# Optimization experiments

Measured on AMD Instinct MI355X. Metric: run time of the kernel, lower is better.

Reference implementation:

```python
import jax, jax.numpy as jnp
import numpy as np

D = 256        # d_model
DL = 256       # d_latent
S = 2048       # seq_len
B = 8          # batches
F = 8192       # facts per batch (padded)
MAXPOS = 4096
MAXPRED = 1024
NROLE = 64 + 2 # role_emb rows


def setup_inputs() -> dict:
    key = jax.random.key(0)
    ks = jax.random.split(key, 16)
    def nrm(k, shape, s=0.02):
        return jax.random.normal(k, shape, jnp.float32) * s
    return {
        "pos_emb": nrm(ks[0], (MAXPOS, D)),
        "pred_emb": nrm(ks[1], (MAXPRED, D)),
        "role_emb": nrm(ks[2], (NROLE, D)),
        "w1": nrm(ks[3], (3 * D, 2 * D)), "b1": jnp.zeros((2 * D,), jnp.float32),
        "w2": nrm(ks[4], (2 * D, D)),     "b2": jnp.zeros((D,), jnp.float32),
        "ln_g": jnp.ones((D,), jnp.float32), "ln_b": jnp.zeros((D,), jnp.float32),
        "lw1": nrm(ks[5], (D, DL)), "lb1": jnp.zeros((DL,), jnp.float32),
        "lw2": nrm(ks[6], (DL, DL)), "lb2": jnp.zeros((DL,), jnp.float32),
        "pred_idx": jax.random.randint(ks[7], (B, F), 0, MAXPRED),
        "a0": jax.random.randint(ks[8], (B, F), 0, S),
        "a1": jax.random.randint(ks[9], (B, F), 0, S),
        "role_idx": jax.random.randint(ks[10], (B, F), 0, NROLE),
        "is_role": jax.random.randint(ks[11], (B, F), 0, 2).astype(jnp.int32),
        "add_rev": jax.random.randint(ks[12], (B, F), 0, 2).astype(jnp.int32),
        "mask": jax.random.randint(ks[13], (B, F), 0, 2).astype(jnp.int32),
        "seq_len": S,
    }


def reference(pos_emb, pred_emb, role_emb, w1, b1, w2, b2, ln_g, ln_b,
              lw1, lb1, lw2, lb2,
              pred_idx, a0, a1, role_idx, is_role, add_rev, mask, seq_len):
    nodes = pos_emb[:seq_len]                 # [S, D] shared across batches
    pe = pred_emb[pred_idx]                   # [B, F, D]
    n0 = nodes[a0]                            # [B, F, D]
    n1 = nodes[a1]                            # [B, F, D]
    re = role_emb[role_idx]                   # [B, F, D]

    role_b = is_role.astype(bool)
    valid = mask.astype(bool)

    third = jnp.where(role_b[..., None], re, n1)
    x_fwd = jnp.concatenate([n0, pe, third], axis=-1)   # [B, F, 3D]
    x_rev = jnp.concatenate([n1, pe, n0], axis=-1)      # [B, F, 3D]

    def mlp(x):
        h = jax.nn.gelu(x @ w1 + b1, approximate=False)
        return h @ w2 + b2

    msg_fwd = mlp(x_fwd)                      # [B, F, D]
    msg_rev = mlp(x_rev)                      # [B, F, D]

    w_fwd = valid[..., None].astype(msg_fwd.dtype)
    w_rev = (valid & (~role_b) & add_rev.astype(bool))[..., None].astype(msg_rev.dtype)
    tgt_fwd = jnp.where(role_b, a0, a1)       # role msgs go to tok=a0, binary to a1

    def scat(msg, idx, w):
        return jax.ops.segment_sum(msg * w, idx, num_segments=seq_len)

    agg = jax.vmap(scat)(msg_fwd, tgt_fwd, w_fwd)
    agg = agg + jax.vmap(scat)(msg_rev, a0, w_rev)      # [B, S, D]

    x = nodes[None, :, :] + agg
    mu = jnp.mean(x, axis=-1, keepdims=True)
    var = jnp.mean(jnp.square(x - mu), axis=-1, keepdims=True)
    x = (x - mu) / jnp.sqrt(var + 1e-5) * ln_g + ln_b   # LayerNorm

    pooled = jnp.mean(x, axis=1)              # [B, D]
    h = jax.nn.gelu(pooled @ lw1 + lb1, approximate=False)
    return h @ lw2 + lb2                      # [B, DL]
```

## Files before the change

### kernel.cpp

```cpp
#include <hip/hip_runtime.h>
#include <hip/hip_bf16.h>
#include <cstdint>

#define S_LEN 2048
#define DIM   256
#define NBAT  8
#define NFE   8192
#define NEDGE (NBAT*NFE)
#define HID   512
#define INDIM 768

#define OFF_AGG   0u
#define OFF_POOL  16777216u
#define OFF_CNT   16785408u
#define OFF_NODES 16785664u
#define OFF_PRED  17834240u
#define OFF_ROLE  18358528u
#define OFF_W1P   18392576u
#define OFF_W2P   19179008u
#define OFF_FWD   19441152u
#define OFF_REV   19703296u
#define ZERO_BYTES 16785664u

typedef short bshort8 __attribute__((ext_vector_type(8)));
typedef float floatx4 __attribute__((ext_vector_type(4)));

__device__ __forceinline__ float gelu_f(float x) {
  return 0.5f * x * (1.0f + erff(x * 0.70710678118654752f));
}
__device__ __forceinline__ ushort f2bf(float v) {
  __hip_bfloat16 h = __float2bfloat16(v);
  return *reinterpret_cast<ushort*>(&h);
}

__global__ void prep_tables(const float* __restrict__ pos, const float* __restrict__ pred,
                            const float* __restrict__ role,
                            ushort* __restrict__ nodesT, ushort* __restrict__ predT,
                            ushort* __restrict__ roleT) {
  int i = blockIdx.x * blockDim.x + threadIdx.x;
  const int NN = S_LEN * DIM;
  const int NP = 1024 * DIM;
  if (i < NN) nodesT[i] = f2bf(pos[i]);
  else if (i < NN + NP) { int j = i - NN; predT[j] = f2bf(pred[j]); }
  else { int j = i - NN - NP; if (j < 66 * DIM) roleT[j] = f2bf(role[j]); }
}

__global__ void prep_w(const float* __restrict__ w1, const float* __restrict__ w2,
                       ushort* __restrict__ W1p, ushort* __restrict__ W2p) {
  int i = blockIdx.x * blockDim.x + threadIdx.x;
  const int N1 = INDIM * HID;
  if (i < N1) {
    int k = i >> 9, n = i & 511;
    W1p[(((k >> 3) << 9) + n) * 8 + (k & 7)] = f2bf(w1[i]);
  } else {
    int j = i - N1;
    int k = j >> 8, n = j & 255;
    W2p[(((k >> 3) << 8) + n) * 8 + (k & 7)] = f2bf(w2[j]);
  }
}

__global__ void build_lists(const int* __restrict__ mask, const int* __restrict__ is_role,
                            const int* __restrict__ add_rev,
                            int* __restrict__ fwd, int* __restrict__ rev, int* __restrict__ cnt) {
  int e = blockIdx.x * blockDim.x + threadIdx.x;
  if (e >= NEDGE) return;
  if (mask[e]) {
    int p = atomicAdd(&cnt[0], 1);
    fwd[p] = e;
    if (!is_role[e] && add_rev[e]) {
      int q = atomicAdd(&cnt[1], 1);
      rev[q] = e;
    }
  }
}

#define XSTR 1552
#define HSTR 1040
__global__ __launch_bounds__(512, 1)
void mlp_kernel(const int* __restrict__ cnt, const int* __restrict__ fwd, const int* __restrict__ rev,
                const int* __restrict__ a0, const int* __restrict__ a1,
                const int* __restrict__ pred_idx, const int* __restrict__ role_idx,
                const int* __restrict__ is_role,
                const ushort* __restrict__ nodesT, const ushort* __restrict__ predT,
                const ushort* __restrict__ roleT,
                const ushort* __restrict__ W1p, const ushort* __restrict__ W2p,
                const float* __restrict__ b1, const float* __restrict__ b2,
                float* __restrict__ agg) {
  __shared__ __align__(16) unsigned char smem[64 * XSTR];
  __shared__ int ltgt[64];
  __shared__ int lbat[64];

  const int tid = threadIdx.x;
  const int nf = cnt[0], nr = cnt[1];
  const int total = nf + nr;
  const int row0 = blockIdx.x * 64;
  if (row0 >= total) return;

  if (tid < 64) {
    int grow = row0 + tid;
    int tgt = -1, bb = 0;
    if (grow < total) {
      bool rv = grow >= nf;
      int e = rv ? rev[grow - nf] : fwd[grow];
      bb = e >> 13;
      tgt = rv ? a0[e] : (is_role[e] ? a0[e] : a1[e]);
    }
    ltgt[tid] = tgt; lbat[tid] = bb;
  }
  {
    int r = tid >> 3, sub = tid & 7;
    int grow = row0 + r;
    const ushort *s0, *s1, *s2;
    if (grow < total) {
      bool rv = grow >= nf;
      int e = rv ? rev[grow - nf] : fwd[grow];
      int A0 = a0[e], A1 = a1[e], pi = pred_idx[e];
      s1 = predT + pi * DIM;
      if (rv) { s0 = nodesT + A1 * DIM; s2 = nodesT + A0 * DIM; }
      else {
        s0 = nodesT + A0 * DIM;
        s2 = is_role[e] ? (roleT + role_idx[e] * DIM) : (nodesT + A1 * DIM);
      }
    } else { s0 = s1 = s2 = nodesT; }
    unsigned char* xrow = smem + r * XSTR;
#pragma unroll
    for (int c = 0; c < 12; ++c) {
      int ch = sub * 12 + c;
      int col = ch * 8;
      const ushort* src = (col < 256) ? (s0 + col) : (col < 512) ? (s1 + col - 256) : (s2 + col - 512);
      *reinterpret_cast<uint4*>(xrow + ch * 16) = *reinterpret_cast<const uint4*>(src);
    }
  }
  __syncthreads();

  const int lane = tid & 63, wave = tid >> 6;
  const int wm = wave >> 2, wn = wave & 3;
  const int l15 = lane & 15, kb = lane >> 4;

  floatx4 acc1[2][8];
#pragma unroll
  for (int fm = 0; fm < 2; ++fm)
#pragma unroll
    for (int fn = 0; fn < 8; ++fn) acc1[fm][fn] = (floatx4){0.f, 0.f, 0.f, 0.f};

  for (int k0 = 0; k0 < INDIM; k0 += 32) {
    bshort8 av[2];
#pragma unroll
    for (int fm = 0; fm < 2; ++fm)
      av[fm] = *reinterpret_cast<const bshort8*>(smem + (wm * 32 + fm * 16 + l15) * XSTR + (k0 + kb * 8) * 2);
    const ushort* wp = W1p + (((k0 >> 3) + kb) * 512 + wn * 128 + l15) * 8;
#pragma unroll
    for (int fn = 0; fn < 8; ++fn) {
      bshort8 bv = *reinterpret_cast<const bshort8*>(wp + fn * 128);
      acc1[0][fn] = __builtin_amdgcn_mfma_f32_16x16x32_bf16(av[0], bv, acc1[0][fn], 0, 0, 0);
      acc1[1][fn] = __builtin_amdgcn_mfma_f32_16x16x32_bf16(av[1], bv, acc1[1][fn], 0, 0, 0);
    }
  }
  __syncthreads();

#pragma unroll
  for (int fn = 0; fn < 8; ++fn) {
    int n = wn * 128 + fn * 16 + l15;
    float bias = b1[n];
#pragma unroll
    for (int fm = 0; fm < 2; ++fm) {
#pragma unroll
      for (int rg = 0; rg < 4; ++rg) {
        int m = wm * 32 + fm * 16 + kb * 4 + rg;
        float v = gelu_f(acc1[fm][fn][rg] + bias);
        *reinterpret_cast<ushort*>(smem + m * HSTR + n * 2) = f2bf(v);
      }
    }
  }
  __syncthreads();

  floatx4 acc2[2][4];
#pragma unroll
  for (int fm = 0; fm < 2; ++fm)
#pragma unroll
    for (int fn = 0; fn < 4; ++fn) acc2[fm][fn] = (floatx4){0.f, 0.f, 0.f, 0.f};

  for (int k0 = 0; k0 < HID; k0 += 32) {
    bshort8 av[2];
#pragma unroll
    for (int fm = 0; fm < 2; ++fm)
      av[fm] = *reinterpret_cast<const bshort8*>(smem + (wm * 32 + fm * 16 + l15) * HSTR + (k0 + kb * 8) * 2);
    const ushort* wp = W2p + (((k0 >> 3) + kb) * 256 + wn * 64 + l15) * 8;
#pragma unroll
    for (int fn = 0; fn < 4; ++fn) {
      bshort8 bv = *reinterpret_cast<const bshort8*>(wp + fn * 128);
      acc2[0][fn] = __builtin_amdgcn_mfma_f32_16x16x32_bf16(av[0], bv, acc2[0][fn], 0, 0, 0);
      acc2[1][fn] = __builtin_amdgcn_mfma_f32_16x16x32_bf16(av[1], bv, acc2[1][fn], 0, 0, 0);
    }
  }

#pragma unroll
  for (int fn = 0; fn < 4; ++fn) {
    int n = wn * 64 + fn * 16 + l15;
    float bias = b2[n];
#pragma unroll
    for (int fm = 0; fm < 2; ++fm) {
#pragma unroll
      for (int rg = 0; rg < 4; ++rg) {
        int m = wm * 32 + fm * 16 + kb * 4 + rg;
        int tgt = ltgt[m];
        if (tgt >= 0) {
          float v = acc2[fm][fn][rg] + bias;
          unsafeAtomicAdd(&agg[((lbat[m] << 11) + tgt) * DIM + n], v);
        }
      }
    }
  }
}

__global__ void ln_pool(const float* __restrict__ pos, const float* __restrict__ agg,
                        const float* __restrict__ g, const float* __restrict__ be,
                        float* __restrict__ pooled_sum) {
  __shared__ float r2[16];
  const int b = blockIdx.x >> 7;
  const int sb = blockIdx.x & 127;
  const int t = threadIdx.x;
  const float gg = g[t], bb = be[t];
  const int wv = t >> 6;
  float psum = 0.f;
#pragma unroll 1
  for (int i = 0; i < 16; ++i) {
    int s = sb * 16 + i;
    float x = pos[s * DIM + t] + agg[((b << 11) + s) * DIM + t];
    float a = x, q = x * x;
#pragma unroll
    for (int o = 32; o > 0; o >>= 1) { a += __shfl_xor(a, o); q += __shfl_xor(q, o); }
    if ((t & 63) == 0) { r2[wv * 2] = a; r2[wv * 2 + 1] = q; }
    __syncthreads();
    a = r2[0] + r2[2] + r2[4] + r2[6];
    q = r2[1] + r2[3] + r2[5] + r2[7];
    __syncthreads();
    float mu = a * (1.f / 256.f);
    float var = q * (1.f / 256.f) - mu * mu;
    float y = (x - mu) * rsqrtf(var + 1e-5f) * gg + bb;
    psum += y;
  }
  unsafeAtomicAdd(&pooled_sum[(b << 8) + t], psum);
}

__global__ void final_mlp(const float* __restrict__ pooled_sum,
                          const float* __restrict__ lw1, const float* __restrict__ lb1,
                          const float* __restrict__ lw2, const float* __restrict__ lb2,
                          float* __restrict__ out) {
  __shared__ float pl[8 * 256];
  __shared__ float hl[8 * 256];
  const int t = threadIdx.x;
#pragma unroll
  for (int r = 0; r < 8; ++r) pl[r * 256 + t] = pooled_sum[r * 256 + t] * (1.f / 2048.f);
  __syncthreads();
  float acc[8];
#pragma unroll
  for (int r = 0; r < 8; ++r) acc[r] = lb1[t];
  for (int d = 0; d < 256; ++d) {
    float w = lw1[d * 256 + t];
#pragma unroll
    for (int r = 0; r < 8; ++r) acc[r] = fmaf(pl[r * 256 + d], w, acc[r]);
  }
#pragma unroll
  for (int r = 0; r < 8; ++r) hl[r * 256 + t] = gelu_f(acc[r]);
  __syncthreads();
#pragma unroll
  for (int r = 0; r < 8; ++r) acc[r] = lb2[t];
  for (int d = 0; d < 256; ++d) {
    float w = lw2[d * 256 + t];
#pragma unroll
    for (int r = 0; r < 8; ++r) acc[r] = fmaf(hl[r * 256 + d], w, acc[r]);
  }
#pragma unroll
  for (int r = 0; r < 8; ++r) out[r * 256 + t] = acc[r];
}

extern "C" void kernel_launch(void* const* d_in, const int* in_sizes, int n_in,
                              void* d_out, int out_size, void* d_ws, size_t ws_size,
                              hipStream_t stream) {
  const float* pos_emb  = (const float*)d_in[0];
  const float* pred_emb = (const float*)d_in[1];
  const float* role_emb = (const float*)d_in[2];
  const float* w1   = (const float*)d_in[3];
  const float* b1   = (const float*)d_in[4];
  const float* w2   = (const float*)d_in[5];
  const float* b2   = (const float*)d_in[6];
  const float* ln_g = (const float*)d_in[7];
  const float* ln_b = (const float*)d_in[8];
  const float* lw1  = (const float*)d_in[9];
  const float* lb1  = (const float*)d_in[10];
  const float* lw2  = (const float*)d_in[11];
  const float* lb2  = (const float*)d_in[12];
  const int* pred_idx = (const int*)d_in[13];
  const int* a0       = (const int*)d_in[14];
  const int* a1       = (const int*)d_in[15];
  const int* role_idx = (const int*)d_in[16];
  const int* is_role  = (const int*)d_in[17];
  const int* add_rev  = (const int*)d_in[18];
  const int* mask     = (const int*)d_in[19];

  unsigned char* ws = (unsigned char*)d_ws;
  float*  agg    = (float*)(ws + OFF_AGG);
  float*  pooled = (float*)(ws + OFF_POOL);
  int*    cnt    = (int*)(ws + OFF_CNT);
  ushort* nodesT = (ushort*)(ws + OFF_NODES);
  ushort* predT  = (ushort*)(ws + OFF_PRED);
  ushort* roleT  = (ushort*)(ws + OFF_ROLE);
  ushort* W1p    = (ushort*)(ws + OFF_W1P);
  ushort* W2p    = (ushort*)(ws + OFF_W2P);
  int*    fwd    = (int*)(ws + OFF_FWD);
  int*    rev    = (int*)(ws + OFF_REV);

  hipMemsetAsync(ws, 0, ZERO_BYTES, stream);
  prep_tables<<<3138, 256, 0, stream>>>(pos_emb, pred_emb, role_emb, nodesT, predT, roleT);
  prep_w<<<2048, 256, 0, stream>>>(w1, w2, W1p, W2p);
  build_lists<<<256, 256, 0, stream>>>(mask, is_role, add_rev, fwd, rev, cnt);
  mlp_kernel<<<2048, 512, 0, stream>>>(cnt, fwd, rev, a0, a1, pred_idx, role_idx, is_role,
                                       nodesT, predT, roleT, W1p, W2p, b1, b2, agg);
  ln_pool<<<1024, 256, 0, stream>>>(pos_emb, agg, ln_g, ln_b, pooled);
  final_mlp<<<1, 256, 0, stream>>>(pooled, lw1, lb1, lw2, lb2, (float*)d_out);
}
```

Before: 324.7 us.

## Fuse prep kernels, stream MLP inputs from global, raise occupancy, parallelize final MLP

Merges the memset, table conversion and weight packing into one prep kernel with vectorised conversion. The MLP kernel stops staging the gathered input rows in shared memory and instead loads bf16 fragments straight from the concatenated tables with one-step prefetch. It swaps MFMA operand order so output rows map to lanes, which gives vectorised bias/GELU stores and per-row scatter atomics. It also shrinks shared memory and raises launch bounds to 4 blocks per CU, and spreads the final MLP across 8 blocks. Occupancy gains may be limited by accumulator register pressure, and direct global gathers may cost more latency than the old LDS staging.

```diff
diff --git a/kernel.cpp b/kernel.cpp
--- a/kernel.cpp
+++ b/kernel.cpp
@@ -5,8 +5,7 @@
 #define S_LEN 2048
 #define DIM   256
 #define NBAT  8
-#define NFE   8192
-#define NEDGE (NBAT*NFE)
+#define NEDGE 65536
 #define HID   512
 #define INDIM 768
 
@@ -24,6 +23,7 @@
 
 typedef short bshort8 __attribute__((ext_vector_type(8)));
 typedef float floatx4 __attribute__((ext_vector_type(4)));
+typedef ushort ushort4v __attribute__((ext_vector_type(4)));
 
 __device__ __forceinline__ float gelu_f(float x) {
   return 0.5f * x * (1.0f + erff(x * 0.70710678118654752f));
@@ -33,29 +33,43 @@
   return *reinterpret_cast<ushort*>(&h);
 }
 
-__global__ void prep_tables(const float* __restrict__ pos, const float* __restrict__ pred,
-                            const float* __restrict__ role,
-                            ushort* __restrict__ nodesT, ushort* __restrict__ predT,
-                            ushort* __restrict__ roleT) {
+#define Z4 1049104
+#define T4 200832
+#define WN 524288
+__global__ void prep_all(const float* __restrict__ pos, const float* __restrict__ pred,
+                         const float* __restrict__ role,
+                         const float* __restrict__ w1, const float* __restrict__ w2,
+                         unsigned char* __restrict__ ws) {
   int i = blockIdx.x * blockDim.x + threadIdx.x;
-  const int NN = S_LEN * DIM;
-  const int NP = 1024 * DIM;
-  if (i < NN) nodesT[i] = f2bf(pos[i]);
-  else if (i < NN + NP) { int j = i - NN; predT[j] = f2bf(pred[j]); }
-  else { int j = i - NN - NP; if (j < 66 * DIM) roleT[j] = f2bf(role[j]); }
-}
-
-__global__ void prep_w(const float* __restrict__ w1, const float* __restrict__ w2,
-                       ushort* __restrict__ W1p, ushort* __restrict__ W2p) {
-  int i = blockIdx.x * blockDim.x + threadIdx.x;
-  const int N1 = INDIM * HID;
-  if (i < N1) {
-    int k = i >> 9, n = i & 511;
-    W1p[(((k >> 3) << 9) + n) * 8 + (k & 7)] = f2bf(w1[i]);
-  } else {
-    int j = i - N1;
-    int k = j >> 8, n = j & 255;
-    W2p[(((k >> 3) << 8) + n) * 8 + (k & 7)] = f2bf(w2[j]);
+  if (i < Z4) {
+    reinterpret_cast<float4*>(ws)[i] = float4{0.f, 0.f, 0.f, 0.f};
+    return;
+  }
+  i -= Z4;
+  if (i < T4) {
+    const int NN4 = 131072, NP4 = 65536;
+    float4 v;
+    if (i < NN4) v = reinterpret_cast<const float4*>(pos)[i];
+    else if (i < NN4 + NP4) v = reinterpret_cast<const float4*>(pred)[i - NN4];
+    else v = reinterpret_cast<const float4*>(role)[i - NN4 - NP4];
+    ushort4v h;
+    h.x = f2bf(v.x); h.y = f2bf(v.y); h.z = f2bf(v.z); h.w = f2bf(v.w);
+    *reinterpret_cast<ushort4v*>((ushort*)(ws + OFF_NODES) + (i << 2)) = h;
+    return;
+  }
+  i -= T4;
+  if (i < WN) {
+    ushort* W1p = (ushort*)(ws + OFF_W1P);
+    ushort* W2p = (ushort*)(ws + OFF_W2P);
+    const int N1 = INDIM * HID;
+    if (i < N1) {
+      int k = i >> 9, n = i & 511;
+      W1p[(((k >> 3) << 9) + n) * 8 + (k & 7)] = f2bf(w1[i]);
+    } else {
+      int j = i - N1;
+      int k = j >> 8, n = j & 255;
+      W2p[(((k >> 3) << 8) + n) * 8 + (k & 7)] = f2bf(w2[j]);
+    }
   }
 }
 
@@ -74,21 +88,20 @@
   }
 }
 
-#define XSTR 1552
-#define HSTR 1040
-__global__ __launch_bounds__(512, 1)
+#define HSTR_E 520
+__global__ __launch_bounds__(512, 4)
 void mlp_kernel(const int* __restrict__ cnt, const int* __restrict__ fwd, const int* __restrict__ rev,
                 const int* __restrict__ a0, const int* __restrict__ a1,
                 const int* __restrict__ pred_idx, const int* __restrict__ role_idx,
                 const int* __restrict__ is_role,
-                const ushort* __restrict__ nodesT, const ushort* __restrict__ predT,
-                const ushort* __restrict__ roleT,
+                const ushort* __restrict__ T,
                 const ushort* __restrict__ W1p, const ushort* __restrict__ W2p,
                 const float* __restrict__ b1, const float* __restrict__ b2,
                 float* __restrict__ agg) {
-  __shared__ __align__(16) unsigned char smem[64 * XSTR];
+  __shared__ ushort Hs[64 * HSTR_E];
   __shared__ int ltgt[64];
   __shared__ int lbat[64];
+  __shared__ uint loff[64][3];
 
   const int tid = threadIdx.x;
   const int nf = cnt[0], nr = cnt[1];
@@ -98,44 +111,30 @@
 
   if (tid < 64) {
     int grow = row0 + tid;
-    int tgt = -1, bb = 0;
+    int tgt = -1, bb = 0; uint o0 = 0, o1 = 0, o2 = 0;
     if (grow < total) {
       bool rv = grow >= nf;
       int e = rv ? rev[grow - nf] : fwd[grow];
       bb = e >> 13;
-      tgt = rv ? a0[e] : (is_role[e] ? a0[e] : a1[e]);
+      int A0 = a0[e], A1 = a1[e];
+      o1 = 524288u + ((uint)pred_idx[e] << 8);
+      if (rv)              { o0 = (uint)A1 << 8; o2 = (uint)A0 << 8;                      tgt = A0; }
+      else if (is_role[e]) { o0 = (uint)A0 << 8; o2 = 786432u + ((uint)role_idx[e] << 8); tgt = A0; }
+      else                 { o0 = (uint)A0 << 8; o2 = (uint)A1 << 8;                      tgt = A1; }
     }
     ltgt[tid] = tgt; lbat[tid] = bb;
-  }
-  {
-    int r = tid >> 3, sub = tid & 7;
-    int grow = row0 + r;
-    const ushort *s0, *s1, *s2;
-    if (grow < total) {
-      bool rv = grow >= nf;
-      int e = rv ? rev[grow - nf] : fwd[grow];
-      int A0 = a0[e], A1 = a1[e], pi = pred_idx[e];
-      s1 = predT + pi * DIM;
-      if (rv) { s0 = nodesT + A1 * DIM; s2 = nodesT + A0 * DIM; }
-      else {
-        s0 = nodesT + A0 * DIM;
-        s2 = is_role[e] ? (roleT + role_idx[e] * DIM) : (nodesT + A1 * DIM);
-      }
-    } else { s0 = s1 = s2 = nodesT; }
-    unsigned char* xrow = smem + r * XSTR;
-#pragma unroll
-    for (int c = 0; c < 12; ++c) {
-      int ch = sub * 12 + c;
-      int col = ch * 8;
-      const ushort* src = (col < 256) ? (s0 + col) : (col < 512) ? (s1 + col - 256) : (s2 + col - 512);
-      *reinterpret_cast<uint4*>(xrow + ch * 16) = *reinterpret_cast<const uint4*>(src);
-    }
+    loff[tid][0] = o0; loff[tid][1] = o1; loff[tid][2] = o2;
   }
   __syncthreads();
 
   const int lane = tid & 63, wave = tid >> 6;
   const int wm = wave >> 2, wn = wave & 3;
   const int l15 = lane & 15, kb = lane >> 4;
+  const int m0 = wm * 32 + l15;
+  const int m1 = m0 + 16;
+
+  const uint o00 = loff[m0][0], o01 = loff[m0][1], o02 = loff[m0][2];
+  const uint o10 = loff[m1][0], o11 = loff[m1][1], o12 = loff[m1][2];
 
   floatx4 acc1[2][8];
 #pragma unroll
@@ -143,71 +142,78 @@
 #pragma unroll
     for (int fn = 0; fn < 8; ++fn) acc1[fm][fn] = (floatx4){0.f, 0.f, 0.f, 0.f};
 
+  const int kcb = kb * 8;
+  bshort8 xb0 = *reinterpret_cast<const bshort8*>(T + o00 + kcb);
+  bshort8 xb1 = *reinterpret_cast<const bshort8*>(T + o10 + kcb);
+#pragma unroll 1
   for (int k0 = 0; k0 < INDIM; k0 += 32) {
-    bshort8 av[2];
-#pragma unroll
-    for (int fm = 0; fm < 2; ++fm)
-      av[fm] = *reinterpret_cast<const bshort8*>(smem + (wm * 32 + fm * 16 + l15) * XSTR + (k0 + kb * 8) * 2);
-    const ushort* wp = W1p + (((k0 >> 3) + kb) * 512 + wn * 128 + l15) * 8;
+    int k1 = k0 + 32;
+    uint po0 = (k1 < 256) ? o00 : (k1 < 512) ? o01 : o02;
+    uint po1 = (k1 < 256) ? o10 : (k1 < 512) ? o11 : o12;
+    int kc1 = (k1 & 255) + kcb;
+    bshort8 nx0 = *reinterpret_cast<const bshort8*>(T + po0 + kc1);
+    bshort8 nx1 = *reinterpret_cast<const bshort8*>(T + po1 + kc1);
+
+    const ushort* wp = W1p + ((((k0 >> 3) + kb) << 9) + wn * 128 + l15) * 8;
 #pragma unroll
     for (int fn = 0; fn < 8; ++fn) {
-      bshort8 bv = *reinterpret_cast<const bshort8*>(wp + fn * 128);
-      acc1[0][fn] = __builtin_amdgcn_mfma_f32_16x16x32_bf16(av[0], bv, acc1[0][fn], 0, 0, 0);
-      acc1[1][fn] = __builtin_amdgcn_mfma_f32_16x16x32_bf16(av[1], bv, acc1[1][fn], 0, 0, 0);
+      bshort8 wv = *reinterpret_cast<const bshort8*>(wp + (fn << 7));
+      acc1[0][fn] = __builtin_amdgcn_mfma_f32_16x16x32_bf16(wv, xb0, acc1[0][fn], 0, 0, 0);
+      acc1[1][fn] = __builtin_amdgcn_mfma_f32_16x16x32_bf16(wv, xb1, acc1[1][fn], 0, 0, 0);
+    }
+    xb0 = nx0; xb1 = nx1;
+  }
+
+#pragma unroll
+  for (int fm = 0; fm < 2; ++fm) {
+    int m = fm ? m1 : m0;
+#pragma unroll
+    for (int fn = 0; fn < 8; ++fn) {
+      int n0 = wn * 128 + fn * 16 + kb * 4;
+      float4 bb4 = *reinterpret_cast<const float4*>(b1 + n0);
+      ushort4v hv;
+      hv.x = f2bf(gelu_f(acc1[fm][fn][0] + bb4.x));
+      hv.y = f2bf(gelu_f(acc1[fm][fn][1] + bb4.y));
+      hv.z = f2bf(gelu_f(acc1[fm][fn][2] + bb4.z));
+      hv.w = f2bf(gelu_f(acc1[fm][fn][3] + bb4.w));
+      *reinterpret_cast<ushort4v*>(Hs + m * HSTR_E + n0) = hv;
     }
   }
   __syncthreads();
 
-#pragma unroll
-  for (int fn = 0; fn < 8; ++fn) {
-    int n = wn * 128 + fn * 16 + l15;
-    float bias = b1[n];
-#pragma unroll
-    for (int fm = 0; fm < 2; ++fm) {
-#pragma unroll
-      for (int rg = 0; rg < 4; ++rg) {
-        int m = wm * 32 + fm * 16 + kb * 4 + rg;
-        float v = gelu_f(acc1[fm][fn][rg] + bias);
-        *reinterpret_cast<ushort*>(smem + m * HSTR + n * 2) = f2bf(v);
-      }
-    }
-  }
-  __syncthreads();
-
   floatx4 acc2[2][4];
 #pragma unroll
   for (int fm = 0; fm < 2; ++fm)
 #pragma unroll
     for (int fn = 0; fn < 4; ++fn) acc2[fm][fn] = (floatx4){0.f, 0.f, 0.f, 0.f};
 
+#pragma unroll 1
   for (int k0 = 0; k0 < HID; k0 += 32) {
-    bshort8 av[2];
-#pragma unroll
-    for (int fm = 0; fm < 2; ++fm)
-      av[fm] = *reinterpret_cast<const bshort8*>(smem + (wm * 32 + fm * 16 + l15) * HSTR + (k0 + kb * 8) * 2);
-    const ushort* wp = W2p + (((k0 >> 3) + kb) * 256 + wn * 64 + l15) * 8;
+    bshort8 hb0 = *reinterpret_cast<const bshort8*>(Hs + m0 * HSTR_E + k0 + kcb);
+    bshort8 hb1 = *reinterpret_cast<const bshort8*>(Hs + m1 * HSTR_E + k0 + kcb);
+    const ushort* wp2 = W2p + ((((k0 >> 3) + kb) << 8) + wn * 64 + l15) * 8;
 #pragma unroll
     for (int fn = 0; fn < 4; ++fn) {
-      bshort8 bv = *reinterpret_cast<const bshort8*>(wp + fn * 128);
-      acc2[0][fn] = __builtin_amdgcn_mfma_f32_16x16x32_bf16(av[0], bv, acc2[0][fn], 0, 0, 0);
-      acc2[1][fn] = __builtin_amdgcn_mfma_f32_16x16x32_bf16(av[1], bv, acc2[1][fn], 0, 0, 0);
-    }
-  }
-
-#pragma unroll
-  for (int fn = 0; fn < 4; ++fn) {
-    int n = wn * 64 + fn * 16 + l15;
-    float bias = b2[n];
-#pragma unroll
-    for (int fm = 0; fm < 2; ++fm) {
-#pragma unroll
-      for (int rg = 0; rg < 4; ++rg) {
-        int m = wm * 32 + fm * 16 + kb * 4 + rg;
-        int tgt = ltgt[m];
-        if (tgt >= 0) {
-          float v = acc2[fm][fn][rg] + bias;
-          unsafeAtomicAdd(&agg[((lbat[m] << 11) + tgt) * DIM + n], v);
-        }
+      bshort8 wv = *reinterpret_cast<const bshort8*>(wp2 + (fn << 7));
+      acc2[0][fn] = __builtin_amdgcn_mfma_f32_16x16x32_bf16(wv, hb0, acc2[0][fn], 0, 0, 0);
+      acc2[1][fn] = __builtin_amdgcn_mfma_f32_16x16x32_bf16(wv, hb1, acc2[1][fn], 0, 0, 0);
+    }
+  }
+
+#pragma unroll
+  for (int fm = 0; fm < 2; ++fm) {
+    int m = fm ? m1 : m0;
+    int tgt = ltgt[m];
+    if (tgt >= 0) {
+      float* dst = agg + ((((uint)lbat[m] << 11) + (uint)tgt) << 8);
+#pragma unroll
+      for (int fn = 0; fn < 4; ++fn) {
+        int n0 = wn * 64 + fn * 16 + kb * 4;
+        float4 bb4 = *reinterpret_cast<const float4*>(b2 + n0);
+        unsafeAtomicAdd(dst + n0 + 0, acc2[fm][fn][0] + bb4.x);
+        unsafeAtomicAdd(dst + n0 + 1, acc2[fm][fn][1] + bb4.y);
+        unsafeAtomicAdd(dst + n0 + 2, acc2[fm][fn][2] + bb4.z);
+        unsafeAtomicAdd(dst + n0 + 3, acc2[fm][fn][3] + bb4.w);
       }
     }
   }
@@ -247,32 +253,20 @@
                           const float* __restrict__ lw1, const float* __restrict__ lb1,
                           const float* __restrict__ lw2, const float* __restrict__ lb2,
                           float* __restrict__ out) {
-  __shared__ float pl[8 * 256];
-  __shared__ float hl[8 * 256];
-  const int t = threadIdx.x;
-#pragma unroll
-  for (int r = 0; r < 8; ++r) pl[r * 256 + t] = pooled_sum[r * 256 + t] * (1.f / 2048.f);
+  __shared__ float pl[256];
+  __shared__ float hl[256];
+  const int r = blockIdx.x, t = threadIdx.x;
+  pl[t] = pooled_sum[(r << 8) + t] * (1.f / 2048.f);
   __syncthreads();
-  float acc[8];
-#pragma unroll
-  for (int r = 0; r < 8; ++r) acc[r] = lb1[t];
-  for (int d = 0; d < 256; ++d) {
-    float w = lw1[d * 256 + t];
-#pragma unroll
-    for (int r = 0; r < 8; ++r) acc[r] = fmaf(pl[r * 256 + d], w, acc[r]);
-  }
-#pragma unroll
-  for (int r = 0; r < 8; ++r) hl[r * 256 + t] = gelu_f(acc[r]);
+  float a = lb1[t];
+#pragma unroll 8
+  for (int d = 0; d < 256; ++d) a = fmaf(pl[d], lw1[(d << 8) + t], a);
+  hl[t] = gelu_f(a);
   __syncthreads();
-#pragma unroll
-  for (int r = 0; r < 8; ++r) acc[r] = lb2[t];
-  for (int d = 0; d < 256; ++d) {
-    float w = lw2[d * 256 + t];
-#pragma unroll
-    for (int r = 0; r < 8; ++r) acc[r] = fmaf(hl[r * 256 + d], w, acc[r]);
-  }
-#pragma unroll
-  for (int r = 0; r < 8; ++r) out[r * 256 + t] = acc[r];
+  float o = lb2[t];
+#pragma unroll 8
+  for (int d = 0; d < 256; ++d) o = fmaf(hl[d], lw2[(d << 8) + t], o);
+  out[(r << 8) + t] = o;
 }
 
 extern "C" void kernel_launch(void* const* d_in, const int* in_sizes, int n_in,
@@ -303,20 +297,16 @@
   float*  agg    = (float*)(ws + OFF_AGG);
   float*  pooled = (float*)(ws + OFF_POOL);
   int*    cnt    = (int*)(ws + OFF_CNT);
-  ushort* nodesT = (ushort*)(ws + OFF_NODES);
-  ushort* predT  = (ushort*)(ws + OFF_PRED);
-  ushort* roleT  = (ushort*)(ws + OFF_ROLE);
+  ushort* T      = (ushort*)(ws + OFF_NODES);
   ushort* W1p    = (ushort*)(ws + OFF_W1P);
   ushort* W2p    = (ushort*)(ws + OFF_W2P);
   int*    fwd    = (int*)(ws + OFF_FWD);
   int*    rev    = (int*)(ws + OFF_REV);
 
-  hipMemsetAsync(ws, 0, ZERO_BYTES, stream);
-  prep_tables<<<3138, 256, 0, stream>>>(pos_emb, pred_emb, role_emb, nodesT, predT, roleT);
-  prep_w<<<2048, 256, 0, stream>>>(w1, w2, W1p, W2p);
+  prep_all<<<6931, 256, 0, stream>>>(pos_emb, pred_emb, role_emb, w1, w2, ws);
   build_lists<<<256, 256, 0, stream>>>(mask, is_role, add_rev, fwd, rev, cnt);
   mlp_kernel<<<2048, 512, 0, stream>>>(cnt, fwd, rev, a0, a1, pred_idx, role_idx, is_role,
-                                       nodesT, predT, roleT, W1p, W2p, b1, b2, agg);
+                                       T, W1p, W2p, b1, b2, agg);
   ln_pool<<<1024, 256, 0, stream>>>(pos_emb, agg, ln_g, ln_b, pooled);
-  final_mlp<<<1, 256, 0, stream>>>(pooled, lw1, lb1, lw2, lb2, (float*)d_out);
-}
+  final_mlp<<<8, 256, 0, stream>>>(pooled, lw1, lb1, lw2, lb2, (float*)d_out);
+}
```

After: 374.2 us. 15.3% more time.
